# Optimization experiments

Measured on AMD Instinct MI355X. Metric: run time of the kernel, lower is better.

The kernel has to match this reference:

```python
import jax, jax.numpy as jnp
import numpy as np
from math import sqrt

FMAP = [38, 19, 10, 5, 3, 1]
SCALES = [0.1, 0.2, 0.375, 0.55, 0.725, 0.9]
RATIOS = [[1.0, 2.0, 0.5], [1.0, 2.0, 3.0, 0.5, 0.333], [1.0, 2.0, 3.0, 0.5, 0.333],
          [1.0, 2.0, 3.0, 0.5, 0.333], [1.0, 2.0, 0.5], [1.0, 2.0, 0.5]]
MIN_SCORE = 0.01
MAX_OVERLAP = 0.45
PRE_NMS = 400  # fixed per-class candidate cap (makes NMS jit-compatible)


def make_priors():
    boxes = []
    for k, (fd, s, rs) in enumerate(zip(FMAP, SCALES, RATIOS)):
        for i in range(fd):
            for j in range(fd):
                cx = (j + 0.5) / fd
                cy = (i + 0.5) / fd
                for r in rs:
                    boxes.append([cx, cy, s * sqrt(r), s / sqrt(r)])
                    if r == 1:
                        add = sqrt(s * SCALES[k + 1]) if k + 1 < len(SCALES) else 1.0
                        boxes.append([cx, cy, add, add])
    return np.clip(np.asarray(boxes, np.float32), 0.0, 1.0)  # [8732, 4] cxcywh


def box_iou(a, b):
    # a: [M,4], b: [N,4] in xyxy -> [M,N]
    lt = jnp.maximum(a[:, None, :2], b[None, :, :2])
    rb = jnp.minimum(a[:, None, 2:], b[None, :, 2:])
    wh = jnp.clip(rb - lt, 0.0)
    inter = wh[..., 0] * wh[..., 1]
    area_a = (a[:, 2] - a[:, 0]) * (a[:, 3] - a[:, 1])
    area_b = (b[:, 2] - b[:, 0]) * (b[:, 3] - b[:, 1])
    union = area_a[:, None] + area_b[None, :] - inter
    return inter / jnp.maximum(union, 1e-10)


def _nms_one_class(boxes, scores):
    # boxes: [P,4] xyxy, scores: [P]
    s = jnp.where(scores > MIN_SCORE, scores, -1.0)
    vals, idx = jax.lax.top_k(s, PRE_NMS)          # [PRE]
    cand = boxes[idx]                               # [PRE,4]
    valid = vals > MIN_SCORE
    iou = box_iou(cand, cand)                       # [PRE,PRE]

    def step(sup, i):
        active = valid[i] & ~sup[i]
        new = jnp.where(active, sup | (iou[i] > MAX_OVERLAP), sup)
        new = new.at[i].set(jnp.where(active, False, new[i]))
        return new, None

    sup, _ = jax.lax.scan(step, jnp.zeros(PRE_NMS, bool), jnp.arange(PRE_NMS))
    keep = valid & ~sup
    return cand, jnp.where(keep, vals, -1.0)


def _detect_image(locs, scores, priors, top_k):
    # decode gcxgcy -> cxcywh -> xyxy
    cxcy = locs[:, :2] * priors[:, 2:] / 10.0 + priors[:, :2]
    wh = jnp.exp(locs[:, 2:] / 5.0) * priors[:, 2:]
    boxes = jnp.concatenate([cxcy - wh / 2.0, cxcy + wh / 2.0], axis=-1)  # [P,4]
    probs = jax.nn.softmax(scores, axis=-1)        # [P,C]
    cls_scores = probs[:, 1:].T                     # [C-1, P] (skip background)
    cand_boxes, cand_scores = jax.vmap(lambda s: _nms_one_class(boxes, s))(cls_scores)
    labels = jnp.broadcast_to(jnp.arange(1, probs.shape[1], dtype=jnp.int32)[:, None],
                              cand_scores.shape)
    flat_s = cand_scores.reshape(-1)
    flat_b = cand_boxes.reshape(-1, 4)
    flat_l = labels.reshape(-1)
    top_s, top_i = jax.lax.top_k(flat_s, top_k)
    return flat_b[top_i], flat_l[top_i], top_s


def setup_inputs() -> dict:
    key = jax.random.key(0)
    k1, k2 = jax.random.split(key)
    B, P, C = 8, 8732, 81
    return {
        "predicted_locs": jax.random.normal(k1, (B, P, 4), jnp.float32),
        "predicted_scores": jax.random.normal(k2, (B, P, C), jnp.float32),
        "priors": jnp.asarray(make_priors()),
        "top_k": 200,
    }


def reference(predicted_locs, predicted_scores, priors, top_k):
    # boxes [B,top_k,4], labels [B,top_k] int32, scores [B,top_k]
    # (invalid/padded detections carry score == -1.0)
    return jax.vmap(lambda l, s: _detect_image(l, s, priors, top_k))(
        predicted_locs, predicted_scores)
```

## Files before the change

### kernel.cpp

```cpp
#include <hip/hip_runtime.h>
#include <cstdint>

typedef unsigned long long u64;
typedef unsigned int u32;

#define WPRE 400
#define MIN_SCORE 0.01f
#define MAX_OVERLAP 0.45f
#define INV32 0x407FFFFFu

#define IOU_MID 0x1.CCCCCDp-2

__device__ __forceinline__ u32 f32_key(float f) {
    u32 u = __float_as_uint(f);
    return (f >= 0.0f) ? (u | 0x80000000u) : ~u;
}
__device__ __forceinline__ float key_f32(u32 k) {
    return __uint_as_float((k & 0x80000000u) ? (k ^ 0x80000000u) : ~k);
}

struct SelSt {
    u64 prefix, thr;
    int r, above, shift, nge, done;
    u32 wtot[8];
};

template <int T, typename KF>
__device__ void hist_select64(KF kf, int N, int K, int CAP, u64 bulk,
                              int tid, u32* hist, SelSt* st)
{
    const int lane = tid & 63;
    const int wv = tid >> 6;
    const int nw = T >> 6;
    constexpr int BPT = 1024 / T;

    if (tid == 0) { st->prefix = 0ull; st->r = K; st->above = 0; st->shift = 54; st->done = 0; }
    __syncthreads();

    while (true) {
        const int shift = st->shift;
        const u64 pref = st->prefix;
        const int r = st->r;
        const int above = st->above;
        const bool lvl0 = (shift == 54);
        #pragma unroll
        for (int q = 0; q < BPT; ++q) hist[tid * BPT + q] = 0u;
        __syncthreads();

        const bool useBulk = (bulk != 0ull) && (shift >= 14);
        const u64 bulkHi = bulk >> 14;
        u32 bulkCnt = 0;
        for (int i = tid; i < N; i += T) {
            u64 k;
            if (!kf(i, k)) continue;
            if (!lvl0 && (k >> (shift + 10)) != pref) continue;
            if (useBulk && (k >> 14) == bulkHi) { ++bulkCnt; continue; }
            atomicAdd(&hist[(u32)(k >> shift) & 1023u], 1u);
        }
        if (useBulk) {
            #pragma unroll
            for (int off = 32; off > 0; off >>= 1) bulkCnt += __shfl_down(bulkCnt, off, 64);
            if (lane == 0 && bulkCnt) atomicAdd(&hist[(u32)(bulk >> shift) & 1023u], bulkCnt);
        }
        __syncthreads();

        u32 hloc[BPT], Sarr[BPT];
        u32 run = 0;
        #pragma unroll
        for (int q = BPT - 1; q >= 0; --q) {
            hloc[q] = hist[tid * BPT + q];
            run += hloc[q];
            Sarr[q] = run;
        }
        u32 incl = run;
        #pragma unroll
        for (int off = 1; off < 64; off <<= 1) {
            u32 x = __shfl_down(incl, off, 64);
            incl += (lane + off < 64) ? x : 0u;
        }
        if (lane == 0) st->wtot[wv] = incl;
        __syncthreads();
        u32 wa = 0;
        for (int w2 = wv + 1; w2 < nw; ++w2) wa += st->wtot[w2];
        const u32 suffAbove = wa + (incl - run);

        bool found = false; int fb = 0; u32 fSn = 0, fh = 0;
        #pragma unroll
        for (int q = 0; q < BPT; ++q) {
            u32 S = suffAbove + Sarr[q];
            u32 Sn = S - hloc[q];
            if ((int)S >= r && (int)Sn < r) { found = true; fb = tid * BPT + q; fSn = Sn; fh = hloc[q]; }
        }
        __syncthreads();
        if (found) {
            u64 np = (pref << 10) | (u64)(u32)fb;
            int nab = above + (int)fSn;
            int nge = nab + (int)fh;
            st->prefix = np;
            st->r = r - (int)fSn;
            st->above = nab;
            st->nge = nge;
            st->thr = np << shift;
            st->shift = shift - 10;
            st->done = (nge <= CAP) || (shift == 4);
        }
        __syncthreads();
        if (st->done) break;
    }
}

__global__ __launch_bounds__(256) void decode_softmax_kernel(
    const float* __restrict__ locs, const float* __restrict__ scores,
    const float* __restrict__ priors, float* __restrict__ dec,
    float* __restrict__ probs_t, int P, int C, int NC)
{
    __shared__ float tile[64 * 81];
    __shared__ float mrow[64], srow[64];
    const int b  = blockIdx.y;
    const int p0 = blockIdx.x * 64;
    const int tid = threadIdx.x;
    const int nrows = min(64, P - p0);
    const int n = nrows * C;

    const float* src = scores + ((size_t)b * P + p0) * C;
    for (int idx = tid; idx < n; idx += 256) tile[idx] = src[idx];

    if (tid < nrows) {
        int p = p0 + tid;
        float4 lc = ((const float4*)locs)[(size_t)b * P + p];
        float4 pr = ((const float4*)priors)[p];
        float cx = lc.x * pr.z / 10.0f + pr.x;
        float cy = lc.y * pr.w / 10.0f + pr.y;
        float w  = expf(lc.z / 5.0f) * pr.z;
        float h  = expf(lc.w / 5.0f) * pr.w;
        ((float4*)dec)[(size_t)b * P + p] =
            make_float4(cx - w * 0.5f, cy - h * 0.5f, cx + w * 0.5f, cy + h * 0.5f);
    }
    __syncthreads();

    if (tid < nrows) {
        const float* row = &tile[tid * C];
        float m = row[0];
        for (int cc = 1; cc < C; ++cc) m = fmaxf(m, row[cc]);
        float ss = 0.f;
        for (int cc = 0; cc < C; ++cc) ss += expf(row[cc] - m);
        mrow[tid] = m; srow[tid] = ss;
    }
    __syncthreads();

    for (int idx = tid; idx < 64 * NC; idx += 256) {
        int r  = idx & 63;
        int cc = idx >> 6;
        if (r < nrows) {
            float v = expf(tile[r * C + cc + 1] - mrow[r]) / srow[r];
            probs_t[((size_t)(b * NC + cc)) * P + p0 + r] = v;
        }
    }
}

__global__ __launch_bounds__(512) void select_nms_kernel(
    const float* __restrict__ dec, const float* __restrict__ probs_t,
    float* __restrict__ cand_sc, float* __restrict__ cand_bx,
    int P, int NC)
{
    const int c = blockIdx.x, b = blockIdx.y;
    const int tid = threadIdx.x;
    const int lane = tid & 63;
    const int wv = tid >> 6;
    const int T = 512;

    __shared__ alignas(16) char bufA[8736 * 4];
    u32* skey = (u32*)bufA;
    u64* inw  = (u64*)bufA;
    float4* cbox = (float4*)(bufA + 25088);
    float*  ara  = (float*)(bufA + 32256);
    __shared__ u64 cand[512];
    u32* hist = (u32*)cand;
    __shared__ u64 validm[7], keepm[7];
    __shared__ SelSt st;
    __shared__ int sh_cnt;

    const float* ps = probs_t + ((size_t)(b * NC + c)) * P;

    int P4 = P >> 2;
    for (int i = tid; i < P4; i += T) {
        float4 f4 = ((const float4*)ps)[i];
        skey[i*4+0] = f32_key(f4.x > MIN_SCORE ? f4.x : -1.0f);
        skey[i*4+1] = f32_key(f4.y > MIN_SCORE ? f4.y : -1.0f);
        skey[i*4+2] = f32_key(f4.z > MIN_SCORE ? f4.z : -1.0f);
        skey[i*4+3] = f32_key(f4.w > MIN_SCORE ? f4.w : -1.0f);
    }
    for (int i = (P4 << 2) + tid; i < P; i += T) {
        float f = ps[i];
        skey[i] = f32_key(f > MIN_SCORE ? f : -1.0f);
    }
    if (tid == 0) sh_cnt = 0;
    __syncthreads();

    hist_select64<512>([&](int i, u64& k) {
                           k = ((u64)skey[i] << 32) | (u64)(u32)(~(u32)i);
                           return true;
                       },
                       P, WPRE, 512, ((u64)INV32) << 32, tid, hist, &st);
    const u64 thr = st.thr;

    for (int i = tid; i < P; i += T) {
        u64 k = ((u64)skey[i] << 32) | (u64)(u32)(~(u32)i);
        if (k >= thr) {
            int pos = atomicAdd(&sh_cnt, 1);
            if (pos < 512) cand[pos] = k;
        }
    }
    __syncthreads();
    const int cnt = sh_cnt;
    u64 v = (tid < cnt) ? cand[tid] : 0ull;

    for (int k = 2; k <= 512; k <<= 1) {
        for (int j = k >> 1; j > 0; j >>= 1) {
            u64 p;
            if (j < 64) {
                p = __shfl_xor(v, j, 64);
            } else {
                __syncthreads();
                cand[tid] = v;
                __syncthreads();
                p = cand[tid ^ j];
            }
            bool takeMax = (((tid & k) == 0) == ((tid & j) == 0));
            v = takeMax ? (v > p ? v : p) : (v > p ? p : v);
        }
    }
    __syncthreads();

    float4 mybox = make_float4(0.f, 0.f, 0.f, 0.f);
    float myval = -1.0f;
    if (tid < 448) {
        if (tid < WPRE) {
            myval = key_f32((u32)(v >> 32));
            int p = (int)(~(u32)v);
            mybox = ((const float4*)dec)[(size_t)b * P + p];
        }
        cbox[tid] = mybox;
        ara[tid] = (mybox.z - mybox.x) * (mybox.w - mybox.y);
        u64 mk = __ballot(myval > MIN_SCORE);
        if (lane == 0) validm[tid >> 6] = mk;
    }
    __syncthreads();

    for (int tt = wv; tt < 28; tt += 8) {
        int r = 0, base = 0;
        while (tt - base >= 7 - r) { base += 7 - r; ++r; }
        int w = r + (tt - base);
        int j = (w << 6) + lane;
        float4 bj = cbox[j];
        float aj = ara[j];
        const int i0 = r << 6;
        u32 acc0 = 0u, acc1 = 0u;
        #pragma unroll 16
        for (int q = 0; q < 32; ++q) {
            int i = i0 + q;
            float4 bi = cbox[i];
            float ai = ara[i];
            float lx = fmaxf(bi.x, bj.x);
            float ly = fmaxf(bi.y, bj.y);
            float rx = fminf(bi.z, bj.z);
            float ry = fminf(bi.w, bj.w);
            float ww = fmaxf(rx - lx, 0.f);
            float hh = fmaxf(ry - ly, 0.f);
            float inter = ww * hh;
            float uniC = fmaxf((ai + aj) - inter, 1e-10f);
            bool pred = (double)inter > IOU_MID * (double)uniC;
            acc0 |= pred ? (1u << q) : 0u;
        }
        #pragma unroll 16
        for (int q = 0; q < 32; ++q) {
            int i = i0 + 32 + q;
            float4 bi = cbox[i];
            float ai = ara[i];
            float lx = fmaxf(bi.x, bj.x);
            float ly = fmaxf(bi.y, bj.y);
            float rx = fminf(bi.z, bj.z);
            float ry = fminf(bi.w, bj.w);
            float ww = fmaxf(rx - lx, 0.f);
            float hh = fmaxf(ry - ly, 0.f);
            float inter = ww * hh;
            float uniC = fmaxf((ai + aj) - inter, 1e-10f);
            bool pred = (double)inter > IOU_MID * (double)uniC;
            acc1 |= pred ? (1u << q) : 0u;
        }
        inw[(w * 7 + r) * 64 + lane] = ((u64)acc1 << 32) | acc0;
    }
    __syncthreads();

    if (wv == 0) {
        u64 keep[7];
        #pragma unroll
        for (int w2 = 0; w2 < 7; ++w2) {
            bool alive = ((validm[w2] >> lane) & 1ull) != 0;
            #pragma unroll
            for (int r = 0; r < w2; ++r) {
                u64 inr = inw[(w2 * 7 + r) * 64 + lane];
                alive = alive && ((inr & keep[r]) == 0ull);
            }
            u64 in_self = inw[(w2 * 7 + w2) * 64 + lane];
            u64 inmask = in_self & ((1ull << lane) - 1ull);
            u64 mm = inmask;
            #pragma unroll
            for (int off = 32; off; off >>= 1) mm |= __shfl_xor(mm, off, 64);
            while (mm) {
                int t = __builtin_ctzll(mm);
                mm &= mm - 1ull;
                u64 am = __ballot(alive);
                if ((am >> t) & 1ull)
                    alive = alive && (((inmask >> t) & 1ull) == 0ull);
            }
            u64 fin = __ballot(alive);
            keep[w2] = fin;
            if (lane == 0) keepm[w2] = fin;
        }
    }
    __syncthreads();

    if (tid < WPRE) {
        bool keep = (keepm[tid >> 6] >> (tid & 63)) & 1ull;
        cand_sc[((size_t)(b * NC + c)) * WPRE + tid] = keep ? myval : -1.0f;
        ((float4*)cand_bx)[((size_t)(b * NC + c)) * WPRE + tid] = mybox;
    }
}

__global__ __launch_bounds__(512) void topkA_kernel(
    const float* __restrict__ cand_sc, u64* __restrict__ wsA,
    int NC, int TOPK, int GS, int NG)
{
    const int g = blockIdx.x, b = blockIdx.y;
    const int tid = threadIdx.x;
    const int T = 512;
    const int N = GS;
    const u32 fbase = (u32)(g * GS);

    __shared__ u32 hist[1024];
    __shared__ SelSt st;
    __shared__ int sh_cnt;

    const float* s = cand_sc + (size_t)b * NC * WPRE + (size_t)g * GS;
    u64* outg = wsA + (size_t)(b * NG + g) * 256;

    if (tid == 0) sh_cnt = 0;
    __syncthreads();

    hist_select64<512>([&](int i, u64& k) {
                           k = ((u64)f32_key(s[i]) << 32) | (u64)(u32)(~(fbase + (u32)i));
                           return true;
                       },
                       N, TOPK, 256, ((u64)INV32) << 32, tid, hist, &st);
    const u64 thr = st.thr;

    for (int i = tid; i < N; i += T) {
        u64 k = ((u64)f32_key(s[i]) << 32) | (u64)(u32)(~(fbase + (u32)i));
        if (k >= thr) {
            int pos = atomicAdd(&sh_cnt, 1);
            if (pos < 256) outg[pos] = k;
        }
    }
    __syncthreads();
    int cnt = sh_cnt;
    if (tid < 256 && tid >= cnt) outg[tid] = 0ull;
}

__global__ __launch_bounds__(256) void topkB_kernel(
    const u64* __restrict__ wsA, const float* __restrict__ cand_bx,
    float* __restrict__ out, int NC, int TOPK, int B, int NG)
{
    const int b = blockIdx.x;
    const int tid = threadIdx.x;
    const int T = 256;
    const int N = NG * 256;

    __shared__ u64 keys[2560];
    __shared__ u32 hist[1024];
    u64* cand = (u64*)hist;
    __shared__ SelSt st;
    __shared__ int sh_cnt;

    const u64* src = wsA + (size_t)b * N;
    for (int i = tid; i < N; i += T) keys[i] = src[i];
    if (tid == 0) sh_cnt = 0;
    __syncthreads();

    hist_select64<256>([&](int i, u64& k) { k = keys[i]; return true; },
                       N, TOPK, 256, ((u64)INV32) << 32, tid, hist, &st);
    const u64 thr = st.thr;

    for (int i = tid; i < N; i += T) {
        u64 k = keys[i];
        if (k >= thr) {
            int pos = atomicAdd(&sh_cnt, 1);
            if (pos < 256) cand[pos] = k;
        }
    }
    __syncthreads();
    int cnt = sh_cnt;
    u64 v = (tid < cnt) ? cand[tid] : 0ull;

    for (int k = 2; k <= 256; k <<= 1) {
        for (int j = k >> 1; j > 0; j >>= 1) {
            u64 p;
            if (j < 64) {
                p = __shfl_xor(v, j, 64);
            } else {
                __syncthreads();
                cand[tid] = v;
                __syncthreads();
                p = cand[tid ^ j];
            }
            bool takeMax = (((tid & k) == 0) == ((tid & j) == 0));
            v = takeMax ? (v > p ? v : p) : (v > p ? p : v);
        }
    }

    if (tid < TOPK) {
        float sc = key_f32((u32)(v >> 32));
        int flat = (int)(~(u32)v);
        int cls = flat / WPRE;
        float4 bx = ((const float4*)cand_bx)[(size_t)b * NC * WPRE + flat];
        float* ob = out + ((size_t)(b * TOPK + tid)) * 4;
        ob[0] = bx.x; ob[1] = bx.y; ob[2] = bx.z; ob[3] = bx.w;
        out[(size_t)B * TOPK * 4 + (size_t)b * TOPK + tid] = (float)(cls + 1);
        out[(size_t)B * TOPK * 5 + (size_t)b * TOPK + tid] = sc;
    }
}

extern "C" void kernel_launch(void* const* d_in, const int* in_sizes, int n_in,
                              void* d_out, int out_size, void* d_ws, size_t ws_size,
                              hipStream_t stream) {
    const float* locs   = (const float*)d_in[0];
    const float* scores = (const float*)d_in[1];
    const float* priors = (const float*)d_in[2];

    const int P  = in_sizes[2] / 4;
    const int B  = in_sizes[0] / (4 * P);
    const int C  = in_sizes[1] / (B * P);
    const int NC = C - 1;
    const int TOPK = out_size / (B * 6);
    const int NG = 10;
    const int GS = (NC * WPRE) / NG;

    float* ws      = (float*)d_ws;
    float* dec     = ws;
    float* probs_t = dec + (size_t)B * P * 4;
    float* cand_sc = probs_t + (size_t)B * NC * P;
    float* cand_bx = cand_sc + (size_t)B * NC * WPRE;
    u64*   wsA     = (u64*)(cand_bx + (size_t)B * NC * WPRE * 4);

    dim3 g1((P + 63) / 64, B);
    decode_softmax_kernel<<<g1, 256, 0, stream>>>(locs, scores, priors, dec, probs_t, P, C, NC);

    dim3 g2(NC, B);
    select_nms_kernel<<<g2, 512, 0, stream>>>(dec, probs_t, cand_sc, cand_bx, P, NC);

    dim3 g3(NG, B);
    topkA_kernel<<<g3, 512, 0, stream>>>(cand_sc, wsA, NC, TOPK, GS, NG);
    topkB_kernel<<<dim3(B), 256, 0, stream>>>(wsA, cand_bx, (float*)d_out, NC, TOPK, B, NG);
}
```

Measured before the change: 141.7 us.

## Split per-class candidate selection into chunked blocks before NMS

Per-class top-400 selection over 8732 priors is split across 4 chunk blocks, each keeping 512 padded keys in workspace. A second kernel selects the final 400 from the 2048 chunk keys and runs NMS. This raises parallelism from 640 blocks to 2560 for the selection phase, but adds a kernel launch and workspace traffic. Box areas are now recomputed inline instead of read from shared memory, and the select thresholds' fill values change. The chunked path runs only when the workspace is large enough, otherwise the old fused kernel is used.

New measurement: 143.5 us. Within noise of the previous version (+1.3%).

```diff
diff --git a/kernel.cpp b/kernel.cpp
--- a/kernel.cpp
+++ b/kernel.cpp
@@ -8,6 +8,8 @@
 #define MIN_SCORE 0.01f
 #define MAX_OVERLAP 0.45f
 #define INV32 0x407FFFFFu
+#define CHUNK 2184
+#define NCH 4
 
 #define IOU_MID 0x1.CCCCCDp-2
 
@@ -158,8 +160,58 @@
     }
 }
 
-__global__ __launch_bounds__(512) void select_nms_kernel(
-    const float* __restrict__ dec, const float* __restrict__ probs_t,
+__global__ __launch_bounds__(256) void chunk_select_kernel(
+    const float* __restrict__ probs_t, u64* __restrict__ chunkk,
+    int P, int NC)
+{
+    const int c = blockIdx.x, b = blockIdx.y, z = blockIdx.z;
+    const int tid = threadIdx.x;
+    const int T = 256;
+    const int off = z * CHUNK;
+    const int PC = min(CHUNK, P - off);
+
+    __shared__ u32 skey[CHUNK];
+    __shared__ u32 hist[1024];
+    __shared__ SelSt st;
+    __shared__ int sh_cnt;
+
+    const float* ps = probs_t + ((size_t)(b * NC + c)) * P + off;
+    u64* outk = chunkk + ((size_t)(b * NC + c) * NCH + z) * 512;
+
+    const int PC4 = PC >> 2;
+    for (int i = tid; i < PC4; i += T) {
+        float4 f4 = ((const float4*)ps)[i];
+        skey[i*4+0] = f32_key(f4.x > MIN_SCORE ? f4.x : -1.0f);
+        skey[i*4+1] = f32_key(f4.y > MIN_SCORE ? f4.y : -1.0f);
+        skey[i*4+2] = f32_key(f4.z > MIN_SCORE ? f4.z : -1.0f);
+        skey[i*4+3] = f32_key(f4.w > MIN_SCORE ? f4.w : -1.0f);
+    }
+    if (tid == 0) sh_cnt = 0;
+    __syncthreads();
+
+    hist_select64<256>([&](int i, u64& k) {
+                           k = ((u64)skey[i] << 32) | (u64)(u32)(~(u32)(off + i));
+                           return true;
+                       },
+                       PC, WPRE, 512, (((u64)INV32) << 32) | 0xFFFFFFFFull,
+                       tid, hist, &st);
+    const u64 thr = st.thr;
+
+    for (int i = tid; i < PC; i += T) {
+        u64 k = ((u64)skey[i] << 32) | (u64)(u32)(~(u32)(off + i));
+        if (k >= thr) {
+            int pos = atomicAdd(&sh_cnt, 1);
+            if (pos < 512) outk[pos] = k;
+        }
+    }
+    __syncthreads();
+    const int cnt = sh_cnt;
+    for (int s = cnt + tid; s < 512; s += T)
+        outk[s] = (((u64)INV32) << 32) | (u64)(u32)(~(u32)(P + z * 512 + s));
+}
+
+__global__ __launch_bounds__(512) void nms_chunked_kernel(
+    const float* __restrict__ dec, const u64* __restrict__ chunkk,
     float* __restrict__ cand_sc, float* __restrict__ cand_bx,
     int P, int NC)
 {
@@ -170,42 +222,27 @@
     const int T = 512;
 
     __shared__ alignas(16) char bufA[8736 * 4];
-    u32* skey = (u32*)bufA;
+    u64* keys2 = (u64*)bufA;
     u64* inw  = (u64*)bufA;
     float4* cbox = (float4*)(bufA + 25088);
-    float*  ara  = (float*)(bufA + 32256);
     __shared__ u64 cand[512];
     u32* hist = (u32*)cand;
     __shared__ u64 validm[7], keepm[7];
     __shared__ SelSt st;
     __shared__ int sh_cnt;
 
-    const float* ps = probs_t + ((size_t)(b * NC + c)) * P;
-
-    int P4 = P >> 2;
-    for (int i = tid; i < P4; i += T) {
-        float4 f4 = ((const float4*)ps)[i];
-        skey[i*4+0] = f32_key(f4.x > MIN_SCORE ? f4.x : -1.0f);
-        skey[i*4+1] = f32_key(f4.y > MIN_SCORE ? f4.y : -1.0f);
-        skey[i*4+2] = f32_key(f4.z > MIN_SCORE ? f4.z : -1.0f);
-        skey[i*4+3] = f32_key(f4.w > MIN_SCORE ? f4.w : -1.0f);
-    }
-    for (int i = (P4 << 2) + tid; i < P; i += T) {
-        float f = ps[i];
-        skey[i] = f32_key(f > MIN_SCORE ? f : -1.0f);
-    }
+    const u64* src = chunkk + (size_t)(b * NC + c) * NCH * 512;
+    for (int i = tid; i < NCH * 512; i += T) keys2[i] = src[i];
     if (tid == 0) sh_cnt = 0;
     __syncthreads();
 
-    hist_select64<512>([&](int i, u64& k) {
-                           k = ((u64)skey[i] << 32) | (u64)(u32)(~(u32)i);
-                           return true;
-                       },
-                       P, WPRE, 512, ((u64)INV32) << 32, tid, hist, &st);
+    hist_select64<512>([&](int i, u64& k) { k = keys2[i]; return true; },
+                       NCH * 512, WPRE, 512, (((u64)INV32) << 32) | 0xFFFFFFFFull,
+                       tid, hist, &st);
     const u64 thr = st.thr;
 
-    for (int i = tid; i < P; i += T) {
-        u64 k = ((u64)skey[i] << 32) | (u64)(u32)(~(u32)i);
+    for (int i = tid; i < NCH * 512; i += T) {
+        u64 k = keys2[i];
         if (k >= thr) {
             int pos = atomicAdd(&sh_cnt, 1);
             if (pos < 512) cand[pos] = k;
@@ -241,7 +278,6 @@
             mybox = ((const float4*)dec)[(size_t)b * P + p];
         }
         cbox[tid] = mybox;
-        ara[tid] = (mybox.z - mybox.x) * (mybox.w - mybox.y);
         u64 mk = __ballot(myval > MIN_SCORE);
         if (lane == 0) validm[tid >> 6] = mk;
     }
@@ -253,14 +289,14 @@
         int w = r + (tt - base);
         int j = (w << 6) + lane;
         float4 bj = cbox[j];
-        float aj = ara[j];
+        float aj = (bj.z - bj.x) * (bj.w - bj.y);
         const int i0 = r << 6;
         u32 acc0 = 0u, acc1 = 0u;
         #pragma unroll 16
         for (int q = 0; q < 32; ++q) {
             int i = i0 + q;
             float4 bi = cbox[i];
-            float ai = ara[i];
+            float ai = (bi.z - bi.x) * (bi.w - bi.y);
             float lx = fmaxf(bi.x, bj.x);
             float ly = fmaxf(bi.y, bj.y);
             float rx = fminf(bi.z, bj.z);
@@ -276,7 +312,7 @@
         for (int q = 0; q < 32; ++q) {
             int i = i0 + 32 + q;
             float4 bi = cbox[i];
-            float ai = ara[i];
+            float ai = (bi.z - bi.x) * (bi.w - bi.y);
             float lx = fmaxf(bi.x, bj.x);
             float ly = fmaxf(bi.y, bj.y);
             float rx = fminf(bi.z, bj.z);
@@ -328,6 +364,175 @@
     }
 }
 
+__global__ __launch_bounds__(512) void select_nms_kernel(
+    const float* __restrict__ dec, const float* __restrict__ probs_t,
+    float* __restrict__ cand_sc, float* __restrict__ cand_bx,
+    int P, int NC)
+{
+    const int c = blockIdx.x, b = blockIdx.y;
+    const int tid = threadIdx.x;
+    const int lane = tid & 63;
+    const int wv = tid >> 6;
+    const int T = 512;
+
+    __shared__ alignas(16) char bufA[8736 * 4];
+    u32* skey = (u32*)bufA;
+    u64* inw  = (u64*)bufA;
+    float4* cbox = (float4*)(bufA + 25088);
+    __shared__ u64 cand[512];
+    u32* hist = (u32*)cand;
+    __shared__ u64 validm[7], keepm[7];
+    __shared__ SelSt st;
+    __shared__ int sh_cnt;
+
+    const float* ps = probs_t + ((size_t)(b * NC + c)) * P;
+
+    int P4 = P >> 2;
+    for (int i = tid; i < P4; i += T) {
+        float4 f4 = ((const float4*)ps)[i];
+        skey[i*4+0] = f32_key(f4.x > MIN_SCORE ? f4.x : -1.0f);
+        skey[i*4+1] = f32_key(f4.y > MIN_SCORE ? f4.y : -1.0f);
+        skey[i*4+2] = f32_key(f4.z > MIN_SCORE ? f4.z : -1.0f);
+        skey[i*4+3] = f32_key(f4.w > MIN_SCORE ? f4.w : -1.0f);
+    }
+    for (int i = (P4 << 2) + tid; i < P; i += T) {
+        float f = ps[i];
+        skey[i] = f32_key(f > MIN_SCORE ? f : -1.0f);
+    }
+    if (tid == 0) sh_cnt = 0;
+    __syncthreads();
+
+    hist_select64<512>([&](int i, u64& k) {
+                           k = ((u64)skey[i] << 32) | (u64)(u32)(~(u32)i);
+                           return true;
+                       },
+                       P, WPRE, 512, (((u64)INV32) << 32) | 0xFFFFFFFFull,
+                       tid, hist, &st);
+    const u64 thr = st.thr;
+
+    for (int i = tid; i < P; i += T) {
+        u64 k = ((u64)skey[i] << 32) | (u64)(u32)(~(u32)i);
+        if (k >= thr) {
+            int pos = atomicAdd(&sh_cnt, 1);
+            if (pos < 512) cand[pos] = k;
+        }
+    }
+    __syncthreads();
+    const int cnt = sh_cnt;
+    u64 v = (tid < cnt) ? cand[tid] : 0ull;
+
+    for (int k = 2; k <= 512; k <<= 1) {
+        for (int j = k >> 1; j > 0; j >>= 1) {
+            u64 p;
+            if (j < 64) {
+                p = __shfl_xor(v, j, 64);
+            } else {
+                __syncthreads();
+                cand[tid] = v;
+                __syncthreads();
+                p = cand[tid ^ j];
+            }
+            bool takeMax = (((tid & k) == 0) == ((tid & j) == 0));
+            v = takeMax ? (v > p ? v : p) : (v > p ? p : v);
+        }
+    }
+    __syncthreads();
+
+    float4 mybox = make_float4(0.f, 0.f, 0.f, 0.f);
+    float myval = -1.0f;
+    if (tid < 448) {
+        if (tid < WPRE) {
+            myval = key_f32((u32)(v >> 32));
+            int p = (int)(~(u32)v);
+            mybox = ((const float4*)dec)[(size_t)b * P + p];
+        }
+        cbox[tid] = mybox;
+        u64 mk = __ballot(myval > MIN_SCORE);
+        if (lane == 0) validm[tid >> 6] = mk;
+    }
+    __syncthreads();
+
+    for (int tt = wv; tt < 28; tt += 8) {
+        int r = 0, base = 0;
+        while (tt - base >= 7 - r) { base += 7 - r; ++r; }
+        int w = r + (tt - base);
+        int j = (w << 6) + lane;
+        float4 bj = cbox[j];
+        float aj = (bj.z - bj.x) * (bj.w - bj.y);
+        const int i0 = r << 6;
+        u32 acc0 = 0u, acc1 = 0u;
+        #pragma unroll 16
+        for (int q = 0; q < 32; ++q) {
+            int i = i0 + q;
+            float4 bi = cbox[i];
+            float ai = (bi.z - bi.x) * (bi.w - bi.y);
+            float lx = fmaxf(bi.x, bj.x);
+            float ly = fmaxf(bi.y, bj.y);
+            float rx = fminf(bi.z, bj.z);
+            float ry = fminf(bi.w, bj.w);
+            float ww = fmaxf(rx - lx, 0.f);
+            float hh = fmaxf(ry - ly, 0.f);
+            float inter = ww * hh;
+            float uniC = fmaxf((ai + aj) - inter, 1e-10f);
+            bool pred = (double)inter > IOU_MID * (double)uniC;
+            acc0 |= pred ? (1u << q) : 0u;
+        }
+        #pragma unroll 16
+        for (int q = 0; q < 32; ++q) {
+            int i = i0 + 32 + q;
+            float4 bi = cbox[i];
+            float ai = (bi.z - bi.x) * (bi.w - bi.y);
+            float lx = fmaxf(bi.x, bj.x);
+            float ly = fmaxf(bi.y, bj.y);
+            float rx = fminf(bi.z, bj.z);
+            float ry = fminf(bi.w, bj.w);
+            float ww = fmaxf(rx - lx, 0.f);
+            float hh = fmaxf(ry - ly, 0.f);
+            float inter = ww * hh;
+            float uniC = fmaxf((ai + aj) - inter, 1e-10f);
+            bool pred = (double)inter > IOU_MID * (double)uniC;
+            acc1 |= pred ? (1u << q) : 0u;
+        }
+        inw[(w * 7 + r) * 64 + lane] = ((u64)acc1 << 32) | acc0;
+    }
+    __syncthreads();
+
+    if (wv == 0) {
+        u64 keep[7];
+        #pragma unroll
+        for (int w2 = 0; w2 < 7; ++w2) {
+            bool alive = ((validm[w2] >> lane) & 1ull) != 0;
+            #pragma unroll
+            for (int r = 0; r < w2; ++r) {
+                u64 inr = inw[(w2 * 7 + r) * 64 + lane];
+                alive = alive && ((inr & keep[r]) == 0ull);
+            }
+            u64 in_self = inw[(w2 * 7 + w2) * 64 + lane];
+            u64 inmask = in_self & ((1ull << lane) - 1ull);
+            u64 mm = inmask;
+            #pragma unroll
+            for (int off = 32; off; off >>= 1) mm |= __shfl_xor(mm, off, 64);
+            while (mm) {
+                int t = __builtin_ctzll(mm);
+                mm &= mm - 1ull;
+                u64 am = __ballot(alive);
+                if ((am >> t) & 1ull)
+                    alive = alive && (((inmask >> t) & 1ull) == 0ull);
+            }
+            u64 fin = __ballot(alive);
+            keep[w2] = fin;
+            if (lane == 0) keepm[w2] = fin;
+        }
+    }
+    __syncthreads();
+
+    if (tid < WPRE) {
+        bool keep = (keepm[tid >> 6] >> (tid & 63)) & 1ull;
+        cand_sc[((size_t)(b * NC + c)) * WPRE + tid] = keep ? myval : -1.0f;
+        ((float4*)cand_bx)[((size_t)(b * NC + c)) * WPRE + tid] = mybox;
+    }
+}
+
 __global__ __launch_bounds__(512) void topkA_kernel(
     const float* __restrict__ cand_sc, u64* __restrict__ wsA,
     int NC, int TOPK, int GS, int NG)
@@ -352,7 +557,9 @@
                            k = ((u64)f32_key(s[i]) << 32) | (u64)(u32)(~(fbase + (u32)i));
                            return true;
                        },
-                       N, TOPK, 256, ((u64)INV32) << 32, tid, hist, &st);
+                       N, TOPK, 256,
+                       (((u64)INV32) << 32) | (u64)(u32)(~fbase),
+                       tid, hist, &st);
     const u64 thr = st.thr;
 
     for (int i = tid; i < N; i += T) {
@@ -388,7 +595,8 @@
     __syncthreads();
 
     hist_select64<256>([&](int i, u64& k) { k = keys[i]; return true; },
-                       N, TOPK, 256, ((u64)INV32) << 32, tid, hist, &st);
+                       N, TOPK, 256, (((u64)INV32) << 32) | 0xFFFFFFFFull,
+                       tid, hist, &st);
     const u64 thr = st.thr;
 
     for (int i = tid; i < N; i += T) {
@@ -450,13 +658,26 @@
     float* probs_t = dec + (size_t)B * P * 4;
     float* cand_sc = probs_t + (size_t)B * NC * P;
     float* cand_bx = cand_sc + (size_t)B * NC * WPRE;
-    u64*   wsA     = (u64*)(cand_bx + (size_t)B * NC * WPRE * 4);
+    float* base_end = cand_bx + (size_t)B * NC * WPRE * 4;
+    u64*   chunkk  = (u64*)base_end;
+    u64*   wsA     = chunkk;
+
+    const size_t need_chunked =
+        ((size_t)(base_end - ws)) * 4 + (size_t)B * NC * NCH * 512 * 8;
+    const bool chunked = (ws_size >= need_chunked);
 
     dim3 g1((P + 63) / 64, B);
     decode_softmax_kernel<<<g1, 256, 0, stream>>>(locs, scores, priors, dec, probs_t, P, C, NC);
 
-    dim3 g2(NC, B);
-    select_nms_kernel<<<g2, 512, 0, stream>>>(dec, probs_t, cand_sc, cand_bx, P, NC);
+    if (chunked) {
+        dim3 g2a(NC, B, NCH);
+        chunk_select_kernel<<<g2a, 256, 0, stream>>>(probs_t, chunkk, P, NC);
+        dim3 g2b(NC, B);
+        nms_chunked_kernel<<<g2b, 512, 0, stream>>>(dec, chunkk, cand_sc, cand_bx, P, NC);
+    } else {
+        dim3 g2(NC, B);
+        select_nms_kernel<<<g2, 512, 0, stream>>>(dec, probs_t, cand_sc, cand_bx, P, NC);
+    }
 
     dim3 g3(NG, B);
     topkA_kernel<<<g3, 512, 0, stream>>>(cand_sc, wsA, NC, TOPK, GS, NG);
```
